# Performance work log

Measured on AMD Instinct MI355X. Metric: run time of the kernel, lower is better.

## Reference

```python
import jax, jax.numpy as jnp
import numpy as np

KER = 8

def _gelu(x):
    return jax.nn.gelu(x, approximate=False)

def _conv3x3(x, w, b):
    y = jax.lax.conv_general_dilated(x, w, (1, 1), 'SAME',
                                     dimension_numbers=('NCHW', 'OIHW', 'NCHW'))
    return y + b[None, :, None, None]

def _unfold(x):
    # F.unfold(kernel=8, stride=8): [B,C,H,W] -> [B, C*64, L], C-major then kh,kw
    B, C, H, W = x.shape
    Hb, Wb = H // KER, W // KER
    p = x.reshape(B, C, Hb, KER, Wb, KER).transpose(0, 1, 3, 5, 2, 4)
    return p.reshape(B, C * KER * KER, Hb * Wb)

def _fold(cols, H, W):
    # inverse of _unfold (non-overlapping patches)
    B, CK, L = cols.shape
    C = CK // (KER * KER)
    Hb, Wb = H // KER, W // KER
    p = cols.reshape(B, C, KER, KER, Hb, Wb).transpose(0, 1, 4, 2, 5, 3)
    return p.reshape(B, C, H, W)

def _bn(x, g, b, eps=1e-5):
    # train-mode BatchNorm1d on [B, C, L]: stats over (B, L) per channel
    m = x.mean(axis=(0, 2), keepdims=True)
    v = x.var(axis=(0, 2), keepdims=True)
    return (x - m) * jax.lax.rsqrt(v + eps) * g[None, :, None] + b[None, :, None]


def setup_inputs() -> dict:
    key = jax.random.key(0)
    ks = jax.random.split(key, 10)
    ind, d, hid = 64, 1024, 256
    f = lambda k, s: jax.random.normal(k, s, dtype=jnp.float32) * 0.02
    return {
        'feat': jax.random.normal(ks[0], (4, ind, 256, 256), dtype=jnp.float32),
        'w_enc': f(ks[1], (ind, ind, 3, 3)), 'b_enc': jnp.zeros((ind,), jnp.float32),
        'w_k': f(ks[2], (ind, ind, 3, 3)), 'b_k': jnp.zeros((ind,), jnp.float32),
        'w_v': f(ks[3], (ind, ind, 3, 3)), 'b_v': jnp.zeros((ind,), jnp.float32),
        'fcq_w': f(ks[4], (d, ind * KER * KER)), 'fcq_b': jnp.zeros((d,), jnp.float32),
        'fck_w': f(ks[5], (d, ind * KER * KER)), 'fck_b': jnp.zeros((d,), jnp.float32),
        'bnq_g': jnp.ones((d,), jnp.float32), 'bnq_b': jnp.zeros((d,), jnp.float32),
        'bnk_g': jnp.ones((d,), jnp.float32), 'bnk_b': jnp.zeros((d,), jnp.float32),
        'ff1_w': f(ks[6], (hid, ind)), 'ff1_b': jnp.zeros((hid,), jnp.float32),
        'ff2_w': f(ks[7], (ind, hid)), 'ff2_b': jnp.zeros((ind,), jnp.float32),
    }


def reference(feat, w_enc, b_enc, w_k, b_k, w_v, b_v,
              fcq_w, fcq_b, fck_w, fck_b, bnq_g, bnq_b, bnk_g, bnk_b,
              ff1_w, ff1_b, ff2_w, ff2_b):
    B, C, H, W = feat.shape
    fk = _gelu(_conv3x3(feat, w_k, b_k))
    fv = _gelu(_conv3x3(feat, w_v, b_v))
    refer = _gelu(_conv3x3(feat, w_enc, b_enc))
    q_un = _unfold(refer).transpose(0, 2, 1)   # [B, L, C*64]
    k_un = _unfold(fk).transpose(0, 2, 1)
    v_un = _unfold(fv).transpose(0, 2, 1)
    q = jnp.einsum('blc,dc->bld', q_un, fcq_w) + fcq_b
    q = _bn(q.transpose(0, 2, 1), bnq_g, bnq_b).transpose(0, 2, 1)  # [B, L, 1024]
    k = jnp.einsum('blc,dc->bld', k_un, fck_w) + fck_b
    k = _bn(k.transpose(0, 2, 1), bnk_g, bnk_b).transpose(0, 2, 1)
    scores = jnp.einsum('bld,bmd->blm', q, k) / jnp.sqrt(jnp.float32(q.shape[2]))
    attn = jax.nn.softmax(scores, axis=2)
    out = jnp.einsum('blm,bmc->blc', attn, v_un).transpose(0, 2, 1)  # [B, C*64, L]
    out = _fold(out, H, W)
    h = _gelu(jnp.einsum('bchw,oc->bohw', out, ff1_w) + ff1_b[None, :, None, None])
    h = _gelu(jnp.einsum('bchw,oc->bohw', h, ff2_w) + ff2_b[None, :, None, None])
    return h + feat
```

## Files before the change

### kernel.cpp

```cpp
#include <hip/hip_runtime.h>

typedef unsigned short u16;
typedef float f4 __attribute__((ext_vector_type(4)));
typedef float f32x4 __attribute__((ext_vector_type(4)));
typedef short bf16x8 __attribute__((ext_vector_type(8)));
typedef u16 u16x8 __attribute__((ext_vector_type(8)));
typedef u16 u16x4 __attribute__((ext_vector_type(4)));

__device__ __forceinline__ u16 f2bf(float f){
  unsigned u = __float_as_uint(f);
  u = (u + 0x7FFFu + ((u>>16)&1u)) >> 16;
  return (u16)u;
}
__device__ __forceinline__ float bf2f(u16 u){
  return __uint_as_float(((unsigned)u)<<16);
}
__device__ __forceinline__ float gelu_f(float x){
  float y = 1.5957691216057308f*(x + 0.044715f*x*x*x);
  y = fminf(y, 30.0f);
  float t = __expf(y);
  float r = __builtin_amdgcn_rcpf(t + 1.0f);
  return 0.5f*x*(1.0f + (t - 1.0f)*r);
}

typedef __attribute__((address_space(1))) const unsigned int as1_cuint;
typedef __attribute__((address_space(3))) unsigned int as3_uint;
__device__ __forceinline__ void gload_lds16(const void* g, void* l){
  __builtin_amdgcn_global_load_lds((as1_cuint*)g, (as3_uint*)l, 16, 0, 0);
}

__global__ __launch_bounds__(256) void to_nhwc(
    const float* __restrict__ F, u16* __restrict__ O)
{
  __shared__ float tile[64][65];
  const int t = threadIdx.x, b = blockIdx.y;
  const long px0 = (long)blockIdx.x*64;
  const float* Fb = F + (long)b*64*65536;
  #pragma unroll
  for (int i = 0; i < 4; ++i){
    const int ch = (t>>4) + i*16;
    const int pxo = (t&15)*4;
    f4 v = *(const f4*)&Fb[(long)ch*65536 + px0 + pxo];
    tile[ch][pxo]=v[0]; tile[ch][pxo+1]=v[1]; tile[ch][pxo+2]=v[2]; tile[ch][pxo+3]=v[3];
  }
  __syncthreads();
  const int px = t & 63, ch0 = (t>>6)*16;
  u16x8 o0, o1;
  #pragma unroll
  for (int j = 0; j < 8; ++j){ o0[j]=f2bf(tile[ch0+j][px]); o1[j]=f2bf(tile[ch0+8+j][px]); }
  u16* Ob = O + ((long)b*65536 + px0 + px)*64 + ch0;
  *(u16x8*)Ob = o0; *(u16x8*)(Ob+8) = o1;
}

__global__ __launch_bounds__(256) void prep_all(
    const float* __restrict__ we, const float* __restrict__ wk,
    const float* __restrict__ wv, u16* __restrict__ Wt2,
    const float* __restrict__ Wqf, const float* __restrict__ Wkf,
    u16* __restrict__ Oq, u16* __restrict__ Ok,
    const float* __restrict__ W1, const float* __restrict__ W2,
    u16* __restrict__ O1, u16* __restrict__ O2)
{
  const int bb = blockIdx.x, t = threadIdx.x;
  if (bb < 432){
    const int i = bb*256 + t;
    const int cio = i & 31;
    const int t1 = i >> 5;
    const int n  = t1 % 192;
    const int t2 = t1 / 192;
    const int kc = t2 & 1, p = t2 >> 1;
    const int dy = p/3, dx = p - dy*3;
    const int ci = kc*32 + cio;
    const float* W = (n < 64) ? we : (n < 128) ? wk : wv;
    const int co = n & 63;
    Wt2[i] = f2bf(W[((co*64 + ci)*3 + dy)*3 + dx]);
  } else if (bb < 8624){
    const int b2 = bb - 432;
    const int sel = b2 >> 12;
    const long i = ((long)(b2 & 4095)*256 + t)*4;
    const float* s = sel ? Wkf : Wqf;
    u16* d = sel ? Ok : Oq;
    f4 v = *(const f4*)&s[i];
    u16x4 o; o[0]=f2bf(v[0]); o[1]=f2bf(v[1]); o[2]=f2bf(v[2]); o[3]=f2bf(v[3]);
    *(u16x4*)&d[i] = o;
  } else {
    const int b3 = bb - 8624;
    const int sel = b3 >> 4;
    const long i = ((long)(b3 & 15)*256 + t)*4;
    const float* s = sel ? W2 : W1;
    u16* d = sel ? O2 : O1;
    f4 v = *(const f4*)&s[i];
    u16x4 o; o[0]=f2bf(v[0]); o[1]=f2bf(v[1]); o[2]=f2bf(v[2]); o[3]=f2bf(v[3]);
    *(u16x4*)&d[i] = o;
  }
}

__global__ __launch_bounds__(512,2) void conv_mfma(
    const u16* __restrict__ X, const u16* __restrict__ Wt2,
    const float* __restrict__ be, const float* __restrict__ bk, const float* __restrict__ bv,
    u16* __restrict__ Aq, u16* __restrict__ Ak, u16* __restrict__ Vl)
{
  __shared__ __align__(16) u16 smem[24576];
  const int t = threadIdx.x, lane = t & 63, wvi = t >> 6;
  const int bx = blockIdx.x, by = blockIdx.y, b = blockIdx.z;
  const int x0 = bx*16, y0 = by*8;
  const u16* Xb = X + (long)b*4194304;

  #pragma unroll
  for (int j = 0; j < 3; ++j){
    const int id = t + j*512;
    if (id < 1440){
      const int row = id / 144, rem = id - row*144, col = rem >> 3, ck = rem & 7;
      const int y = y0 - 1 + row, x = x0 - 1 + col;
      int4 v = {0,0,0,0};
      if ((unsigned)y < 256u && (unsigned)x < 256u)
        v = *(const int4*)(Xb + ((long)y*256 + x)*64 + ck*8);
      *(int4*)&smem[((row*18 + col)*8 + (ck ^ (col&7)))*8] = v;
    }
  }
  __syncthreads();

  const int wm4 = (wvi>>2)*4;
  const int wn  = (wvi&3)*48;
  const int fr = lane & 15, fo = lane >> 4;
  f32x4 acc[4][3] = {};

  #pragma unroll
  for (int dy = 0; dy < 3; ++dy)
  #pragma unroll
  for (int dx = 0; dx < 3; ++dx){
    const int p = dy*3 + dx;
    #pragma unroll
    for (int kc = 0; kc < 2; ++kc){
      bf16x8 af[4], bfv[3];
      const u16* wp = Wt2 + ((long)(p*2 + kc)*192 + wn + fr)*32 + fo*8;
      #pragma unroll
      for (int ni = 0; ni < 3; ++ni)
        bfv[ni] = *(const bf16x8*)(wp + ni*16*32);
      #pragma unroll
      for (int mi = 0; mi < 4; ++mi){
        const int row = wm4 + mi + dy;
        const int col = fr + dx;
        af[mi] = *(const bf16x8*)&smem[((row*18 + col)*8 + ((kc*4+fo) ^ (col&7)))*8];
      }
      #pragma unroll
      for (int mi = 0; mi < 4; ++mi)
        #pragma unroll
        for (int ni = 0; ni < 3; ++ni)
          acc[mi][ni] = __builtin_amdgcn_mfma_f32_16x16x32_bf16(af[mi], bfv[ni], acc[mi][ni], 0, 0, 0);
    }
  }
  __syncthreads();

  const int c0 = fo*4;
  const int lloc = c0 >> 3, kw0 = c0 & 7;
  #pragma unroll
  for (int ni = 0; ni < 3; ++ni){
    const int n = wn + ni*16 + fr;
    const int mat = n >> 6, co = n & 63;
    const float bias = (mat==0) ? be[co] : (mat==1) ? bk[co] : bv[co];
    #pragma unroll
    for (int mi = 0; mi < 4; ++mi){
      const int r = wm4 + mi;
      u16x4 o;
      #pragma unroll
      for (int rg = 0; rg < 4; ++rg) o[rg] = f2bf(gelu_f(acc[mi][ni][rg] + bias));
      const int e = ((mat*2 + lloc)*64 + co)*64 + ((r*8 + kw0) ^ ((co&7)<<3));
      *(u16x4*)&smem[e] = o;
    }
  }
  __syncthreads();

  const int l_lo = by*32 + bx*2;
  const int co_r = t >> 3, sw = (t&7) ^ (co_r&7);
  const int eoff = co_r*64 + sw*8;
  #pragma unroll
  for (int i = 0; i < 6; ++i){
    const int mat = i >> 1, ll = i & 1;
    u16x8 v = *(const u16x8*)&smem[(mat*2 + ll)*4096 + eoff];
    u16* dst = (mat==0 ? Aq : mat==1 ? Ak : Vl)
             + ((long)b*1024 + l_lo + ll)*4096 + t*8;
    *(u16x8*)dst = v;
  }
}

__global__ __launch_bounds__(256) void v_tr(
    const u16* __restrict__ S, u16* __restrict__ D)
{
  __shared__ u16 tl[64][72];
  const int t = threadIdx.x, b = blockIdx.z;
  const int ck0 = blockIdx.x*64, l0 = blockIdx.y*64;
  const u16* Sb = S + (long)b*4194304;
  u16* Db = D + (long)b*4194304;
  #pragma unroll
  for (int j = 0; j < 2; ++j){
    const int li = (t>>3) + j*32, cko = (t&7)*8;
    *(u16x8*)&tl[li][cko] = *(const u16x8*)(Sb + (long)(l0+li)*4096 + ck0 + cko);
  }
  __syncthreads();
  #pragma unroll
  for (int j = 0; j < 2; ++j){
    const int cki = (t>>3) + j*32, lo = (t&7)*8;
    u16x8 v;
    #pragma unroll
    for (int e = 0; e < 8; ++e) v[e] = tl[lo+e][cki];
    *(u16x8*)(Db + (long)(ck0+cki)*1024 + l0 + lo) = v;
  }
}

__device__ __forceinline__ void xcd_map(int gxl, int gyl, int n8l,
                                        int& bx, int& by, int& bz){
  const int s = blockIdx.x + (blockIdx.y<<gxl) + (blockIdx.z<<(gxl+gyl));
  const int orig = ((s & 7) << n8l) + (s >> 3);
  bx = orig & ((1<<gxl)-1);
  by = (orig >> gxl) & ((1<<gyl)-1);
  bz = orig >> (gxl+gyl);
}

__global__ __launch_bounds__(256,4) void gemm_av(
    const u16* __restrict__ A, long sA,
    const u16* __restrict__ B, long sB,
    void* __restrict__ Cv,
    const int M, const int N, const int K,
    const int gxl, const int gyl, const int n8l)
{
  int bx, by, bI;
  xcd_map(gxl, gyl, n8l, bx, by, bI);
  const u16* Ab = A + (long)bI*sA;
  const u16* Bb = B + (long)bI*sB;
  const int m0 = bx*128, n0 = by*128;
  __shared__ __align__(16) u16 As[8192];
  __shared__ __align__(16) u16 Bs[8192];
  const int t = threadIdx.x, lane = t & 63, wv = t >> 6;
  const int wm = (wv>>1)*64, wn = (wv&1)*64;
  const int fr = lane & 15, fo = lane >> 4;
  f32x4 acc[4][4] = {};
  const int c0 = wv*128 + lane, c1 = c0 + 64;
  const u16* Ag0 = Ab + (long)(m0 + (c0>>2))*K + (c0&3)*8;
  const u16* Ag1 = Ab + (long)(m0 + (c1>>2))*K + (c1&3)*8;
  const u16* Bg0 = Bb + (long)(n0 + (c0>>2))*K + (c0&3)*8;
  const u16* Bg1 = Bb + (long)(n0 + (c1>>2))*K + (c1&3)*8;
  const int lo0 = wv*1024;
  gload_lds16(Ag0, &As[lo0]);
  gload_lds16(Ag1, &As[lo0 + 512]);
  gload_lds16(Bg0, &Bs[lo0]);
  gload_lds16(Bg1, &Bs[lo0 + 512]);
  const int nk = K >> 5;
  int cur = 0;
  for (int ki = 0; ki < nk; ++ki){
    __syncthreads();
    if (ki + 1 < nk){
      const int k0 = (ki + 1) << 5;
      const int so = ((cur^1) << 12) + lo0;
      gload_lds16(Ag0 + k0, &As[so]);
      gload_lds16(Ag1 + k0, &As[so + 512]);
      gload_lds16(Bg0 + k0, &Bs[so]);
      gload_lds16(Bg1 + k0, &Bs[so + 512]);
    }
    const int ro = cur << 12;
    bf16x8 af[4], bfv[4];
    #pragma unroll
    for (int i = 0; i < 4; ++i){
      af[i]  = *(const bf16x8*)&As[ro + (wm + i*16 + fr)*32 + fo*8];
      bfv[i] = *(const bf16x8*)&Bs[ro + (wn + i*16 + fr)*32 + fo*8];
    }
    __builtin_amdgcn_s_setprio(1);
    #pragma unroll
    for (int mi = 0; mi < 4; ++mi)
      #pragma unroll
      for (int ni = 0; ni < 4; ++ni)
        acc[mi][ni] = __builtin_amdgcn_mfma_f32_16x16x32_bf16(af[mi], bfv[ni], acc[mi][ni], 0, 0, 0);
    __builtin_amdgcn_s_setprio(0);
    cur ^= 1;
  }
  u16* O = (u16*)Cv;
  #pragma unroll
  for (int mi = 0; mi < 4; ++mi)
    #pragma unroll
    for (int ni = 0; ni < 4; ++ni){
      const int col = n0 + wn + ni*16 + fr;
      const int c = col >> 6, khh = (col>>3)&7, kww = col&7;
      #pragma unroll
      for (int r = 0; r < 4; ++r){
        const int row = m0 + wm + mi*16 + fo*4 + r;
        const int hb = row >> 5, wbb = row & 31;
        O[(((long)bI*65536 + (hb*8+khh)*256 + wbb*8 + kww)<<6) + c] = f2bf(acc[mi][ni][r]);
      }
    }
}

template<int EPI>
__global__ __launch_bounds__(256,2) void gemm_bt128(
    const u16* __restrict__ A, long sA,
    const u16* __restrict__ B, long sB, const int zshB,
    void* __restrict__ Cv, long sC,
    const int M, const int N, const int K,
    float* __restrict__ bnstats,
    const int gxl, const int gyl, const int n8l)
{
  int bx, by, bI;
  xcd_map(gxl, gyl, n8l, bx, by, bI);
  const u16* Ab = A + (long)bI*sA;
  const u16* Bb = B + (long)(bI>>zshB)*sB;
  const int m0 = bx*128, n0 = by*128;
  __shared__ __align__(16) u16 As[16384];
  __shared__ __align__(16) u16 Bs[16384];
  const int t = threadIdx.x, lane = t & 63, wv = t >> 6;
  const int wm = (wv>>1)*64, wn = (wv&1)*64;
  const int fr = lane & 15, fo = lane >> 4;
  f32x4 acc[4][4] = {};
  const int c0 = wv*128 + lane, c1 = c0 + 64;
  const u16* Ag0 = Ab + (long)(m0 + (c0>>2))*K + (c0&3)*8;
  const u16* Ag1 = Ab + (long)(m0 + (c1>>2))*K + (c1&3)*8;
  const u16* Bg0 = Bb + (long)(n0 + (c0>>2))*K + (c0&3)*8;
  const u16* Bg1 = Bb + (long)(n0 + (c1>>2))*K + (c1&3)*8;
#define STAGEH(slot, h, kofs) { \
    u16* a_ = &As[(((slot)*2+(h))<<12) + wv*1024]; \
    u16* b_ = &Bs[(((slot)*2+(h))<<12) + wv*1024]; \
    const int ko_ = (kofs) + 32*(h); \
    gload_lds16(Ag0 + ko_, a_); \
    gload_lds16(Ag1 + ko_, a_ + 512); \
    gload_lds16(Bg0 + ko_, b_); \
    gload_lds16(Bg1 + ko_, b_ + 512); }
  STAGEH(0, 0, 0)
  STAGEH(0, 1, 0)
  const int nk = K >> 6;
  int cur = 0;
  for (int ki = 0; ki < nk; ++ki){
    __syncthreads();
    if (ki + 1 < nk){
      const int k0 = (ki + 1) << 6;
      STAGEH(cur^1, 0, k0)
      STAGEH(cur^1, 1, k0)
    }
    #pragma unroll
    for (int h = 0; h < 2; ++h){
      const int ro = ((cur*2 + h) << 12);
      bf16x8 af[4], bfv[4];
      #pragma unroll
      for (int i = 0; i < 4; ++i){
        af[i]  = *(const bf16x8*)&As[ro + (wm + i*16 + fr)*32 + fo*8];
        bfv[i] = *(const bf16x8*)&Bs[ro + (wn + i*16 + fr)*32 + fo*8];
      }
      __builtin_amdgcn_s_setprio(1);
      #pragma unroll
      for (int mi = 0; mi < 4; ++mi)
        #pragma unroll
        for (int ni = 0; ni < 4; ++ni)
          acc[mi][ni] = __builtin_amdgcn_mfma_f32_16x16x32_bf16(af[mi], bfv[ni], acc[mi][ni], 0, 0, 0);
      __builtin_amdgcn_s_setprio(0);
    }
    cur ^= 1;
  }
#undef STAGEH
  if (EPI == 3){
    u16* Cb = (u16*)Cv + (long)bI*sC;
    #pragma unroll
    for (int mi = 0; mi < 4; ++mi)
      #pragma unroll
      for (int ni = 0; ni < 4; ++ni){
        const int col = n0 + wn + ni*16 + fr;
        #pragma unroll
        for (int r = 0; r < 4; ++r){
          const int row = m0 + wm + mi*16 + fo*4 + r;
          Cb[(long)row*N + col] = f2bf(acc[mi][ni][r]);
        }
      }
  } else {
    u16* Cb = (u16*)Cv + (long)bI*sC;
    #pragma unroll
    for (int mi = 0; mi < 4; ++mi)
      #pragma unroll
      for (int ni = 0; ni < 4; ++ni){
        const int col = n0 + wn + ni*16 + fr;
        const int row0 = m0 + wm + mi*16 + fo*4;
        u16x4 o;
        #pragma unroll
        for (int r = 0; r < 4; ++r) o[r] = f2bf(acc[mi][ni][r]);
        *(u16x4*)&Cb[(long)col*M + row0] = o;
      }
    const int sel = bI >> 2;
    float* sums = bnstats + sel*2048;
    #pragma unroll
    for (int ni = 0; ni < 4; ++ni){
      float s = 0.f, q = 0.f;
      #pragma unroll
      for (int mi = 0; mi < 4; ++mi)
        #pragma unroll
        for (int r = 0; r < 4; ++r){
          const float v = acc[mi][ni][r];
          s += v; q += v*v;
        }
      s += __shfl_xor(s, 16); s += __shfl_xor(s, 32);
      q += __shfl_xor(q, 16); q += __shfl_xor(q, 32);
      if (fo == 0){
        const int col = n0 + wn + ni*16 + fr;
        atomicAdd(&sums[col], s);
        atomicAdd(&sums[1024 + col], q);
      }
    }
  }
}

__global__ __launch_bounds__(256,2) void ff_fused(
    const u16* __restrict__ X, const u16* __restrict__ W1b,
    const float* __restrict__ B1, const u16* __restrict__ W2b,
    const float* __restrict__ B2, const float* __restrict__ F,
    float* __restrict__ OUT)
{
  __shared__ __align__(16) u16 h1s[128*264];
  const int t = threadIdx.x, lane = t & 63, wv = t >> 6;
  const long m0 = (long)blockIdx.x*128;
  const int fr = lane & 15, fo = lane >> 4;

  {
    const int wm = (wv>>1)*64, wn = (wv&1)*128;
    f32x4 acc[4][8] = {};
    #pragma unroll
    for (int kc = 0; kc < 2; ++kc){
      bf16x8 af[4], bf[8];
      #pragma unroll
      for (int mi = 0; mi < 4; ++mi)
        af[mi] = *(const bf16x8*)(X + (m0 + wm + mi*16 + fr)*64 + kc*32 + fo*8);
      #pragma unroll
      for (int ni = 0; ni < 8; ++ni)
        bf[ni] = *(const bf16x8*)(W1b + (long)(wn + ni*16 + fr)*64 + kc*32 + fo*8);
      #pragma unroll
      for (int mi = 0; mi < 4; ++mi)
        #pragma unroll
        for (int ni = 0; ni < 8; ++ni)
          acc[mi][ni] = __builtin_amdgcn_mfma_f32_16x16x32_bf16(af[mi], bf[ni], acc[mi][ni], 0, 0, 0);
    }
    #pragma unroll
    for (int ni = 0; ni < 8; ++ni){
      const int col = wn + ni*16 + fr;
      const float bc = B1[col];
      #pragma unroll
      for (int mi = 0; mi < 4; ++mi){
        const int row0 = wm + mi*16 + fo*4;
        #pragma unroll
        for (int r = 0; r < 4; ++r)
          h1s[(row0 + r)*264 + col] = f2bf(gelu_f(acc[mi][ni][r] + bc));
      }
    }
  }
  __syncthreads();

  {
    const int wm2 = wv*32;
    f4 fres[2][4]; long idxs[2][4];
    #pragma unroll
    for (int mi = 0; mi < 2; ++mi)
      #pragma unroll
      for (int ni = 0; ni < 4; ++ni){
        const int c = ni*16 + fr;
        const long p = m0 + wm2 + mi*16 + fo*4;
        const int b = (int)(p >> 16), pp = (int)(p & 65535);
        idxs[mi][ni] = ((long)(b*64 + c))*65536 + pp;
        fres[mi][ni] = *(const f4*)&F[idxs[mi][ni]];
      }
    f32x4 acc2[2][4] = {};
    for (int k0 = 0; k0 < 256; k0 += 32){
      bf16x8 af2[2], bf2[4];
      #pragma unroll
      for (int mi = 0; mi < 2; ++mi)
        af2[mi] = *(const bf16x8*)&h1s[(wm2 + mi*16 + fr)*264 + k0 + fo*8];
      #pragma unroll
      for (int ni = 0; ni < 4; ++ni)
        bf2[ni] = *(const bf16x8*)(W2b + (long)(ni*16 + fr)*256 + k0 + fo*8);
      #pragma unroll
      for (int mi = 0; mi < 2; ++mi)
        #pragma unroll
        for (int ni = 0; ni < 4; ++ni)
          acc2[mi][ni] = __builtin_amdgcn_mfma_f32_16x16x32_bf16(af2[mi], bf2[ni], acc2[mi][ni], 0, 0, 0);
    }
    #pragma unroll
    for (int ni = 0; ni < 4; ++ni){
      const int c = ni*16 + fr;
      const float bc = B2[c];
      #pragma unroll
      for (int mi = 0; mi < 2; ++mi){
        f4 o;
        #pragma unroll
        for (int r = 0; r < 4; ++r) o[r] = gelu_f(acc2[mi][ni][r] + bc) + fres[mi][ni][r];
        *(f4*)&OUT[idxs[mi][ni]] = o;
      }
    }
  }
}

__global__ void bn_fin2(float* __restrict__ stats,
                        const float* __restrict__ gq, const float* __restrict__ bq,
                        const float* __restrict__ gk, const float* __restrict__ bk)
{
  const int sel = blockIdx.y;
  const int d = blockIdx.x*256 + threadIdx.x;
  if (d >= 1024) return;
  const float* sum   = stats + sel*2048;
  const float* sumsq = sum + 1024;
  const float* g    = sel ? gk : gq;
  const float* beta = sel ? bk : bq;
  const float m  = sum[d]   * (1.f/4096.f);
  const float vv = sumsq[d] * (1.f/4096.f) - m*m;
  const float sc = g[d] * rsqrtf(vv + 1e-5f);
  stats[4096 + sel*2048 + d]        = sc;
  stats[4096 + sel*2048 + 1024 + d] = beta[d] - m*sc;
}

__global__ __launch_bounds__(256) void bn_apply_t(
    const u16* __restrict__ QT, const float* __restrict__ stats,
    u16* __restrict__ Y)
{
  __shared__ u16 tl[64][72];
  const int t = threadIdx.x, zi = blockIdx.z;
  const int d0 = blockIdx.x*64, l0 = blockIdx.y*64;
  const int sel = zi >> 2;
  const u16* S = QT + (long)zi*1048576;
  u16* D = Y + (long)zi*1048576;
  const float* scp = stats + 4096 + sel*2048;
  const float* shp = scp + 1024;
  #pragma unroll
  for (int j = 0; j < 2; ++j){
    const int di = (t>>3) + j*32, lo = (t&7)*8;
    const int d = d0 + di;
    const float sc = scp[d], sh = shp[d];
    u16x8 v = *(const u16x8*)(S + (long)d*1024 + l0 + lo);
    u16x8 o;
    #pragma unroll
    for (int e = 0; e < 8; ++e) o[e] = f2bf(bf2f(v[e])*sc + sh);
    *(u16x8*)&tl[di][lo] = o;
  }
  __syncthreads();
  #pragma unroll
  for (int j = 0; j < 2; ++j){
    const int li = (t>>3) + j*32, dof = (t&7)*8;
    u16x8 v;
    #pragma unroll
    for (int e = 0; e < 8; ++e) v[e] = tl[dof+e][li];
    *(u16x8*)(D + (long)(l0+li)*1024 + d0 + dof) = v;
  }
}

__global__ __launch_bounds__(256) void softmax_w(
    const u16* __restrict__ S, u16* __restrict__ P)
{
  const int wv = threadIdx.x >> 6, lane = threadIdx.x & 63;
  const long row = (long)blockIdx.x*4 + wv;
  const u16* p = S + row*1024 + lane*16;
  u16x8 a = *(const u16x8*)p;
  u16x8 b = *(const u16x8*)(p + 8);
  float v[16];
  #pragma unroll
  for (int j = 0; j < 8; ++j){ v[j] = bf2f(a[j])*0.03125f; v[8+j] = bf2f(b[j])*0.03125f; }
  float mx = v[0];
  #pragma unroll
  for (int j = 1; j < 16; ++j) mx = fmaxf(mx, v[j]);
  #pragma unroll
  for (int o = 1; o < 64; o <<= 1) mx = fmaxf(mx, __shfl_xor(mx, o));
  float sm = 0.f;
  #pragma unroll
  for (int j = 0; j < 16; ++j){ v[j] = __expf(v[j] - mx); sm += v[j]; }
  #pragma unroll
  for (int o = 1; o < 64; o <<= 1) sm += __shfl_xor(sm, o);
  const float inv = 1.0f/sm;
  u16x8 oa, ob;
  #pragma unroll
  for (int j = 0; j < 8; ++j){ oa[j] = f2bf(v[j]*inv); ob[j] = f2bf(v[8+j]*inv); }
  u16* q = P + row*1024 + lane*16;
  *(u16x8*)q = oa; *(u16x8*)(q + 8) = ob;
}

extern "C" void kernel_launch(void* const* d_in, const int* in_sizes, int n_in,
                              void* d_out, int out_size, void* d_ws, size_t ws_size,
                              hipStream_t stream)
{
  const float* feat  = (const float*)d_in[0];
  const float* w_enc = (const float*)d_in[1];
  const float* b_enc = (const float*)d_in[2];
  const float* w_k   = (const float*)d_in[3];
  const float* b_k   = (const float*)d_in[4];
  const float* w_v   = (const float*)d_in[5];
  const float* b_v   = (const float*)d_in[6];
  const float* fcq_w = (const float*)d_in[7];
  const float* fck_w = (const float*)d_in[9];
  const float* bnq_g = (const float*)d_in[11];
  const float* bnq_b = (const float*)d_in[12];
  const float* bnk_g = (const float*)d_in[13];
  const float* bnk_b = (const float*)d_in[14];
  const float* ff1w  = (const float*)d_in[15];
  const float* ff1b  = (const float*)d_in[16];
  const float* ff2w  = (const float*)d_in[17];
  const float* ff2b  = (const float*)d_in[18];

  char* ws = (char*)d_ws;
  u16*   Aq      = (u16*)  (ws);
  u16*   Ak      = (u16*)  (ws + (32ull<<20));
  u16*   Vc      = (u16*)  (ws + (64ull<<20));
  u16*   Wq      = (u16*)  (ws + (96ull<<20));
  u16*   Wk      = (u16*)  (ws + (104ull<<20));
  u16*   q_bf    = (u16*)  (ws + (112ull<<20));
  u16*   k_bf    = (u16*)  (ws + (120ull<<20));
  u16*   qk_rawT = (u16*)  (ws + (128ull<<20));
  u16*   scores  = (u16*)  (ws + (160ull<<20));
  u16*   attn    = (u16*)  (ws + (176ull<<20));
  u16*   out_nhwc= (u16*)  (ws + (184ull<<20));
  u16*   NX      = (u16*)  (ws + (128ull<<20));
  u16*   Vl      = (u16*)  (ws + (160ull<<20));
  u16*   Wt2     = (u16*)  (ws + (216ull<<20));
  float* stats   = (float*)(ws + (217ull<<20));
  u16*   W1b     = (u16*)  (ws + (218ull<<20));
  u16*   W2b     = (u16*)  (ws + (218ull<<20) + 65536);

  hipMemsetAsync(stats, 0, 4096*sizeof(float), stream);

  to_nhwc<<<dim3(1024,4), 256, 0, stream>>>(feat, NX);
  prep_all<<<dim3(8656), 256, 0, stream>>>(w_enc, w_k, w_v, Wt2,
                                           fcq_w, fck_w, Wq, Wk,
                                           ff1w, ff2w, W1b, W2b);
  conv_mfma<<<dim3(16,32,4), 512, 0, stream>>>(NX, Wt2, b_enc, b_k, b_v, Aq, Ak, Vl);
  v_tr<<<dim3(64,16,4), 256, 0, stream>>>(Vl, Vc);

  gemm_bt128<2><<<dim3(8,8,8), 256, 0, stream>>>(Aq, 4194304, Wq, 4194304, 2,
                                                 qk_rawT, 1048576, 1024, 1024, 4096, stats,
                                                 3, 3, 6);

  bn_fin2<<<dim3(4,2), 256, 0, stream>>>(stats, bnq_g, bnq_b, bnk_g, bnk_b);
  bn_apply_t<<<dim3(16,16,8), 256, 0, stream>>>(qk_rawT, stats, q_bf);

  gemm_bt128<3><<<dim3(8,8,4), 256, 0, stream>>>(q_bf, 1048576, k_bf, 1048576, 0,
                                                 scores, 1048576, 1024, 1024, 1024, nullptr,
                                                 3, 3, 5);
  softmax_w<<<dim3(1024), 256, 0, stream>>>(scores, attn);

  gemm_av<<<dim3(8,32,4), 256, 0, stream>>>(attn, 1048576, Vc, 4194304,
                                            out_nhwc, 1024, 4096, 1024,
                                            3, 5, 7);

  ff_fused<<<dim3(2048), 256, 0, stream>>>(out_nhwc, W1b, ff1b, W2b, ff2b,
                                           feat, (float*)d_out);
}
```

Measured before the change: 453.1 us.

## Enlarge attention-value GEMM tiles to 256x256 with 512-thread blocks

The attn×V GEMM moves from 128x128 tiles with 256 threads and K-step 32 to 256x256 tiles with 512 threads (8 waves, each computing 128x64) and K-step 64. Shared memory grows to 128 KB double-buffered, so only one block fits per CU. The intent is more operand reuse per global load and fewer blocks. In exchange the grid drops to 256 blocks, occupancy falls, and register pressure rises with 32 accumulators per wave.

```diff
diff --git a/kernel.cpp b/kernel.cpp
--- a/kernel.cpp
+++ b/kernel.cpp
@@ -216,72 +216,72 @@
   bz = orig >> (gxl+gyl);
 }
 
-__global__ __launch_bounds__(256,4) void gemm_av(
+__global__ __launch_bounds__(512,1) void gemm_av256(
     const u16* __restrict__ A, long sA,
     const u16* __restrict__ B, long sB,
     void* __restrict__ Cv,
-    const int M, const int N, const int K,
+    const int K,
     const int gxl, const int gyl, const int n8l)
 {
   int bx, by, bI;
   xcd_map(gxl, gyl, n8l, bx, by, bI);
   const u16* Ab = A + (long)bI*sA;
   const u16* Bb = B + (long)bI*sB;
-  const int m0 = bx*128, n0 = by*128;
-  __shared__ __align__(16) u16 As[8192];
-  __shared__ __align__(16) u16 Bs[8192];
+  const int m0 = bx*256, n0 = by*256;
+  __shared__ __align__(16) u16 As[32768];
+  __shared__ __align__(16) u16 Bs[32768];
   const int t = threadIdx.x, lane = t & 63, wv = t >> 6;
-  const int wm = (wv>>1)*64, wn = (wv&1)*64;
+  const int wr = wv >> 2, wc = wv & 3;
   const int fr = lane & 15, fo = lane >> 4;
-  f32x4 acc[4][4] = {};
-  const int c0 = wv*128 + lane, c1 = c0 + 64;
-  const u16* Ag0 = Ab + (long)(m0 + (c0>>2))*K + (c0&3)*8;
-  const u16* Ag1 = Ab + (long)(m0 + (c1>>2))*K + (c1&3)*8;
-  const u16* Bg0 = Bb + (long)(n0 + (c0>>2))*K + (c0&3)*8;
-  const u16* Bg1 = Bb + (long)(n0 + (c1>>2))*K + (c1&3)*8;
-  const int lo0 = wv*1024;
-  gload_lds16(Ag0, &As[lo0]);
-  gload_lds16(Ag1, &As[lo0 + 512]);
-  gload_lds16(Bg0, &Bs[lo0]);
-  gload_lds16(Bg1, &Bs[lo0 + 512]);
-  const int nk = K >> 5;
+  f32x4 acc[8][4] = {};
+  const int crow = (t*4) >> 3;
+  (void)crow;
+#define AV_STAGE(buf, kofs) { \
+    _Pragma("unroll") \
+    for (int j = 0; j < 4; ++j){ \
+      const int cg = wv*256 + j*64;             \
+      const int c  = cg + lane; \
+      const int row = c >> 3, col = (c & 7)*8; \
+      gload_lds16(Ab + (long)(m0 + row)*K + (kofs) + col, &As[(buf)*16384 + cg*8]); \
+      gload_lds16(Bb + (long)(n0 + row)*K + (kofs) + col, &Bs[(buf)*16384 + cg*8]); \
+    } }
+  AV_STAGE(0, 0)
+  const int nk = K >> 6;
   int cur = 0;
   for (int ki = 0; ki < nk; ++ki){
     __syncthreads();
-    if (ki + 1 < nk){
-      const int k0 = (ki + 1) << 5;
-      const int so = ((cur^1) << 12) + lo0;
-      gload_lds16(Ag0 + k0, &As[so]);
-      gload_lds16(Ag1 + k0, &As[so + 512]);
-      gload_lds16(Bg0 + k0, &Bs[so]);
-      gload_lds16(Bg1 + k0, &Bs[so + 512]);
-    }
-    const int ro = cur << 12;
-    bf16x8 af[4], bfv[4];
-    #pragma unroll
-    for (int i = 0; i < 4; ++i){
-      af[i]  = *(const bf16x8*)&As[ro + (wm + i*16 + fr)*32 + fo*8];
-      bfv[i] = *(const bf16x8*)&Bs[ro + (wn + i*16 + fr)*32 + fo*8];
-    }
-    __builtin_amdgcn_s_setprio(1);
-    #pragma unroll
-    for (int mi = 0; mi < 4; ++mi)
+    if (ki + 1 < nk) AV_STAGE(cur^1, (ki + 1) << 6)
+    const int ro = cur << 14;
+    #pragma unroll
+    for (int kc = 0; kc < 2; ++kc){
+      bf16x8 af[8], bfv[4];
+      #pragma unroll
+      for (int mi = 0; mi < 8; ++mi)
+        af[mi] = *(const bf16x8*)&As[ro + (wr*128 + mi*16 + fr)*64 + kc*32 + fo*8];
       #pragma unroll
       for (int ni = 0; ni < 4; ++ni)
-        acc[mi][ni] = __builtin_amdgcn_mfma_f32_16x16x32_bf16(af[mi], bfv[ni], acc[mi][ni], 0, 0, 0);
-    __builtin_amdgcn_s_setprio(0);
+        bfv[ni] = *(const bf16x8*)&Bs[ro + (wc*64 + ni*16 + fr)*64 + kc*32 + fo*8];
+      __builtin_amdgcn_s_setprio(1);
+      #pragma unroll
+      for (int mi = 0; mi < 8; ++mi)
+        #pragma unroll
+        for (int ni = 0; ni < 4; ++ni)
+          acc[mi][ni] = __builtin_amdgcn_mfma_f32_16x16x32_bf16(af[mi], bfv[ni], acc[mi][ni], 0, 0, 0);
+      __builtin_amdgcn_s_setprio(0);
+    }
     cur ^= 1;
   }
+#undef AV_STAGE
   u16* O = (u16*)Cv;
   #pragma unroll
-  for (int mi = 0; mi < 4; ++mi)
+  for (int mi = 0; mi < 8; ++mi)
     #pragma unroll
     for (int ni = 0; ni < 4; ++ni){
-      const int col = n0 + wn + ni*16 + fr;
+      const int col = n0 + wc*64 + ni*16 + fr;
       const int c = col >> 6, khh = (col>>3)&7, kww = col&7;
       #pragma unroll
       for (int r = 0; r < 4; ++r){
-        const int row = m0 + wm + mi*16 + fo*4 + r;
+        const int row = m0 + wr*128 + mi*16 + fo*4 + r;
         const int hb = row >> 5, wbb = row & 31;
         O[(((long)bI*65536 + (hb*8+khh)*256 + wbb*8 + kww)<<6) + c] = f2bf(acc[mi][ni][r]);
       }
@@ -631,9 +631,9 @@
                                                  3, 3, 5);
   softmax_w<<<dim3(1024), 256, 0, stream>>>(scores, attn);
 
-  gemm_av<<<dim3(8,32,4), 256, 0, stream>>>(attn, 1048576, Vc, 4194304,
-                                            out_nhwc, 1024, 4096, 1024,
-                                            3, 5, 7);
+  gemm_av256<<<dim3(4,16,4), 512, 0, stream>>>(attn, 1048576, Vc, 4194304,
+                                               out_nhwc, 1024,
+                                               2, 4, 5);
 
   ff_fused<<<dim3(2048), 256, 0, stream>>>(out_nhwc, W1b, ff1b, W2b, ff2b,
                                            feat, (float*)d_out);
```

Result: slower. 462.9 us (+2.2%).
